# Kernel tuning notes

Measured on AMD Instinct MI355X. Metric: run time of the kernel, lower is better.

The kernel has to match this reference:

```python
import jax, jax.numpy as jnp
import numpy as np

B, T, C = 4, 2048, 2048
H, N = 32, 64          # n_head, head_size; H*N == C (n_dim_att == n_dim)
DMIX, DDEC = 32, 64    # hardcoded LoRA dims in module


def setup_inputs() -> dict:
    key = jax.random.key(0)
    ks = jax.random.split(key, 24)
    u = lambda k, s, lo, hi: jax.random.uniform(k, s, jnp.float32, lo, hi)
    g = lambda k, s: jax.random.normal(k, s, jnp.float32) * 0.02
    return {
        'x': jax.random.normal(ks[0], (B, T, C), jnp.float32),
        'shift_state_in': jax.random.normal(ks[1], (B, C), jnp.float32),
        'wkv_state_in': jnp.zeros((B, H, N, N), jnp.float32),
        'time_maa_x': u(ks[2], (C,), 0.0, 1.0),
        'time_maa_r': u(ks[3], (C,), 0.0, 1.0),
        'time_maa_k': u(ks[4], (C,), 0.0, 1.0),
        'time_maa_v': u(ks[5], (C,), 0.0, 1.0),
        'time_maa_w': u(ks[6], (C,), 0.0, 1.0),
        'time_maa_v2': u(ks[7], (C,), 0.0, 1.0),
        'time_maa_w1': u(ks[8], (C, DMIX * 5), -0.01, 0.01),
        'time_maa_w2': u(ks[9], (5, DMIX, C), -0.01, 0.01),
        'time_decay': u(ks[10], (C,), -6.0, -1.0),
        'time_decay_w1': u(ks[11], (C, DDEC), -0.01, 0.01),
        'time_decay_w2': u(ks[12], (DDEC, C), -0.01, 0.01),
        'time_value2_w1': u(ks[13], (C, DDEC), -0.01, 0.01),
        'time_value2_w2': u(ks[14], (DDEC, C), -0.01, 0.01),
        'W_r': g(ks[15], (C, C)),
        'W_k': g(ks[16], (C, C)),
        'W_v': g(ks[17], (C, C)),
        'W_o': g(ks[18], (C, C)),
        'ln_w': jnp.ones((C,), jnp.float32),
        'ln_b': jnp.zeros((C,), jnp.float32),
    }


def _to_heads(a):
    # [B,T,C] -> [T,B,H,N] for time-major scan
    return a.reshape(B, T, H, N).transpose(1, 0, 2, 3)


def reference(x, shift_state_in, wkv_state_in,
              time_maa_x, time_maa_r, time_maa_k, time_maa_v, time_maa_w, time_maa_v2,
              time_maa_w1, time_maa_w2,
              time_decay, time_decay_w1, time_decay_w2,
              time_value2_w1, time_value2_w2,
              W_r, W_k, W_v, W_o, ln_w, ln_b):
    # token shift
    dxprev = jnp.concatenate([shift_state_in[:, None, :], x[:, :-1]], axis=1) - x
    xxx = x + dxprev * time_maa_x
    hmix = jnp.tanh(xxx @ time_maa_w1).reshape(B, T, 5, DMIX)
    mix = jnp.einsum('btfd,fdc->fbtc', hmix, time_maa_w2)  # [5,B,T,C]
    mr, mk, mv, mw, mv2 = mix
    xr = x + dxprev * (time_maa_r + mr)
    xk = x + dxprev * (time_maa_k + mk)
    xv = x + dxprev * (time_maa_v + mv)
    xw = x + dxprev * (time_maa_w + mw)
    xv2 = x + dxprev * (time_maa_v2 + mv2)

    r = xr @ W_r
    k = xk @ W_k
    v = xv @ W_v
    v2 = xv2 @ W_v + jnp.tanh(xv2 @ time_value2_w1) @ time_value2_w2
    w = time_decay + jnp.tanh(xw @ time_decay_w1) @ time_decay_w2
    decay = jnp.exp(-jnp.exp(w))         # per-channel, data-dependent
    k = k * (1.0 - decay)

    rh, kh, vh, dh = _to_heads(r), _to_heads(k), _to_heads(v), _to_heads(decay)

    def step(state, inputs):
        # state: [B,H,N,N] (k-dim x v-dim); u (time_faaaa) is zero in this variant
        r_t, k_t, v_t, d_t = inputs  # each [B,H,N]
        y = jnp.einsum('bhi,bhij->bhj', r_t, state)
        state = state * d_t[..., None] + k_t[..., None] * v_t[..., None, :]
        return state, y

    wkv_state_out, ys = jax.lax.scan(step, wkv_state_in, (rh, kh, vh, dh))
    y = ys.transpose(1, 0, 2, 3).reshape(B, T, C)
    y = y + v2
    # LayerNorm over n_dim_att
    mu = jnp.mean(y, axis=-1, keepdims=True)
    var = jnp.var(y, axis=-1, keepdims=True)
    y = (y - mu) / jnp.sqrt(var + 1e-5) * ln_w + ln_b
    y = y @ W_o
    return y, x[:, -1], wkv_state_out
```

## Files before the change

kernel.cpp:

```cpp
#include <hip/hip_runtime.h>
#include <hip/hip_bf16.h>
#include <cstdio>


typedef __attribute__((ext_vector_type(8))) short bf16x8;
typedef __attribute__((ext_vector_type(4))) float floatx4;

#define T_DIM 2048
#define C_DIM 2048
#define B_DIM 4
#define M_ROWS (B_DIM * T_DIM)

typedef const unsigned int __attribute__((address_space(1)))* gas1_t;
typedef unsigned int __attribute__((address_space(3)))* las3_t;
__device__ __forceinline__ void gl_lds16(const void* g, void* l) {
    __builtin_amdgcn_global_load_lds((gas1_t)g, (las3_t)l, 16, 0, 0);
}

__global__ __launch_bounds__(256) void k_transpose(
    const float* __restrict__ in, void* __restrict__ out,
    int R, int Cin, int to_bf16)
{
    __shared__ float tile[32][33];
    const int tx = threadIdx.x & 31, ty = threadIdx.x >> 5;
    const int cbase = blockIdx.x * 32, rbase = blockIdx.y * 32;
#pragma unroll
    for (int i = 0; i < 4; i++) {
        int r = rbase + ty + i * 8;
        int c = cbase + tx;
        tile[ty + i * 8][tx] = (c < Cin) ? in[(size_t)r * Cin + c] : 0.0f;
    }
    __syncthreads();
    if (to_bf16) {
        __hip_bfloat16* ob = (__hip_bfloat16*)out;
#pragma unroll
        for (int i = 0; i < 4; i++) {
            int c = cbase + ty + i * 8;
            ob[(size_t)c * R + rbase + tx] = __float2bfloat16(tile[tx][ty + i * 8]);
        }
    } else {
        float* of = (float*)out;
#pragma unroll
        for (int i = 0; i < 4; i++) {
            int c = cbase + ty + i * 8;
            of[(size_t)c * R + rbase + tx] = tile[tx][ty + i * 8];
        }
    }
}

__global__ __launch_bounds__(256) void k_xx(
    const float* __restrict__ x, const float* __restrict__ shift,
    const float* __restrict__ tmx,
    __hip_bfloat16* __restrict__ XX, float* __restrict__ xlast)
{
    const int row = blockIdx.x;
    const int b = row >> 11, t = row & 2047;
    const int c0 = threadIdx.x * 8;
    const float* xrow = x + (size_t)row * C_DIM;
    const float* prow = (t == 0) ? (shift + (size_t)b * C_DIM) : (xrow - C_DIM);
    float4 xa = ((const float4*)(xrow + c0))[0];
    float4 xb = ((const float4*)(xrow + c0))[1];
    float4 pa = ((const float4*)(prow + c0))[0];
    float4 pb = ((const float4*)(prow + c0))[1];
    float xv8[8] = {xa.x, xa.y, xa.z, xa.w, xb.x, xb.y, xb.z, xb.w};
    float pv8[8] = {pa.x, pa.y, pa.z, pa.w, pb.x, pb.y, pb.z, pb.w};
    union { bf16x8 v8; __hip_bfloat16 e[8]; } u;
#pragma unroll
    for (int j = 0; j < 8; j++)
        u.e[j] = __float2bfloat16(fmaf(pv8[j] - xv8[j], tmx[c0 + j], xv8[j]));
    *(bf16x8*)(XX + (size_t)row * C_DIM + c0) = u.v8;
    if (t == T_DIM - 1) {
        ((float4*)(xlast + (size_t)b * C_DIM + c0))[0] = xa;
        ((float4*)(xlast + (size_t)b * C_DIM + c0))[1] = xb;
    }
}

__global__ __launch_bounds__(256) void k_gemm_h(
    const __hip_bfloat16* __restrict__ A,
    const __hip_bfloat16* __restrict__ Bt,
    __hip_bfloat16* __restrict__ Hout)
{
    __shared__ __hip_bfloat16 As[64 * 32];
    __shared__ __hip_bfloat16 Bs[256 * 32];
    const int tid = threadIdx.x;
    const int m0 = blockIdx.x * 64;
    const int wave = tid >> 6, lane = tid & 63;
    const int fcol = lane & 15, quad = lane >> 4;
    floatx4 acc[16];
#pragma unroll
    for (int i = 0; i < 16; i++) acc[i] = (floatx4){0.f, 0.f, 0.f, 0.f};

    const int rA = tid >> 2, kcA = (tid & 3) * 8;
    const __hip_bfloat16* gA = A + (size_t)(m0 + rA) * 2048 + kcA;
    __hip_bfloat16* lA = As + tid * 8;
    const __hip_bfloat16* gB[4];
    __hip_bfloat16* lB[4];
#pragma unroll
    for (int s = 0; s < 4; s++) {
        int q = tid + 256 * s;
        gB[s] = Bt + (size_t)(q >> 2) * 2048 + (q & 3) * 8;
        lB[s] = Bs + q * 8;
    }
    for (int kk = 0; kk < 2048; kk += 32) {
        gl_lds16(gA + kk, lA);
#pragma unroll
        for (int s = 0; s < 4; s++) gl_lds16(gB[s] + kk, lB[s]);
        __syncthreads();
        bf16x8 aF = *(const bf16x8*)(As + (wave * 16 + fcol) * 32 + quad * 8);
#pragma unroll
        for (int ni = 0; ni < 16; ni++) {
            bf16x8 bF = *(const bf16x8*)(Bs + (ni * 16 + fcol) * 32 + quad * 8);
            acc[ni] = __builtin_amdgcn_mfma_f32_16x16x32_bf16(aF, bF, acc[ni], 0, 0, 0);
        }
        __syncthreads();
    }
#pragma unroll
    for (int ni = 0; ni < 16; ni++) {
        int col = ni * 16 + fcol;
#pragma unroll
        for (int g = 0; g < 4; g++) {
            int row = m0 + wave * 16 + quad * 4 + g;
            Hout[(size_t)row * 256 + col] = __float2bfloat16(tanhf(acc[ni][g]));
        }
    }
}

__global__ __launch_bounds__(256) void k_gemm_n64(
    const __hip_bfloat16* __restrict__ A,
    const __hip_bfloat16* __restrict__ Bt,
    __hip_bfloat16* __restrict__ G)
{
    __shared__ __hip_bfloat16 As[64 * 32];
    __shared__ __hip_bfloat16 Bs[64 * 32];
    const int tid = threadIdx.x;
    const int m0 = blockIdx.x * 64;
    const int wave = tid >> 6, lane = tid & 63;
    const int fcol = lane & 15, quad = lane >> 4;
    floatx4 acc[4];
#pragma unroll
    for (int i = 0; i < 4; i++) acc[i] = (floatx4){0.f, 0.f, 0.f, 0.f};

    const int r = tid >> 2, kc = (tid & 3) * 8;
    const __hip_bfloat16* gA = A + (size_t)(m0 + r) * 2048 + kc;
    const __hip_bfloat16* gB = Bt + (size_t)r * 2048 + kc;
    __hip_bfloat16* lA = As + tid * 8;
    __hip_bfloat16* lB = Bs + tid * 8;
    for (int kk = 0; kk < 2048; kk += 32) {
        gl_lds16(gA + kk, lA);
        gl_lds16(gB + kk, lB);
        __syncthreads();
        bf16x8 aF = *(const bf16x8*)(As + (wave * 16 + fcol) * 32 + quad * 8);
#pragma unroll
        for (int ni = 0; ni < 4; ni++) {
            bf16x8 bF = *(const bf16x8*)(Bs + (ni * 16 + fcol) * 32 + quad * 8);
            acc[ni] = __builtin_amdgcn_mfma_f32_16x16x32_bf16(aF, bF, acc[ni], 0, 0, 0);
        }
        __syncthreads();
    }
#pragma unroll
    for (int ni = 0; ni < 4; ni++) {
        int col = ni * 16 + fcol;
#pragma unroll
        for (int g = 0; g < 4; g++) {
            int row = m0 + wave * 16 + quad * 4 + g;
            G[(size_t)row * 64 + col] = __float2bfloat16(tanhf(acc[ni][g]));
        }
    }
}

__global__ __launch_bounds__(256) void k_mixfused(
    const float* __restrict__ x, const float* __restrict__ shift,
    const __hip_bfloat16* __restrict__ Hb,
    const __hip_bfloat16* __restrict__ w2T,
    const float* __restrict__ tmr, const float* __restrict__ tmk,
    const float* __restrict__ tmv, const float* __restrict__ tmw,
    const float* __restrict__ tmv2,
    __hip_bfloat16* __restrict__ xr, __hip_bfloat16* __restrict__ xk,
    __hip_bfloat16* __restrict__ xv, __hip_bfloat16* __restrict__ xw,
    __hip_bfloat16* __restrict__ xv2)
{
    __shared__ float          xp[33 * 256];
    __shared__ __hip_bfloat16 Hs[32 * 256];
    __shared__ __hip_bfloat16 mixS[32 * 256];

    const int tid = threadIdx.x;
    const int bid = blockIdx.x;
    const int n0 = (bid & 7) * 256;
    const int m0 = (bid >> 3) * 32;
    const int wave = tid >> 6, lane = tid & 63;
    const int fcol = lane & 15, quad = lane >> 4;
    const int wm = (wave >> 1) * 16, wn = (wave & 1) * 128;

#pragma unroll
    for (int i = 0; i < 8; i++) {
        int row = i * 4 + wave;
        gl_lds16(x + (size_t)(m0 + row) * C_DIM + n0 + lane * 4,
                 xp + (row + 1) * 256 + lane * 4);
    }
    if (wave == 0) {
        const float* src = (m0 & 2047)
            ? (x + (size_t)(m0 - 1) * C_DIM + n0)
            : (shift + (size_t)(m0 >> 11) * C_DIM + n0);
        gl_lds16(src + lane * 4, xp + lane * 4);
    }
#pragma unroll
    for (int i = 0; i < 4; i++) {
        int q = tid + 256 * i;
        gl_lds16(Hb + (size_t)(m0 + (q >> 5)) * 256 + (q & 31) * 8,
                 Hs + (q >> 5) * 256 + (q & 31) * 8);
    }
    asm volatile("s_waitcnt vmcnt(0) lgkmcnt(0)" ::: "memory");
    __builtin_amdgcn_s_barrier();
    __builtin_amdgcn_sched_barrier(0);

    const float* maas[5] = {tmr, tmk, tmv, tmw, tmv2};
    __hip_bfloat16* outs[5] = {xr, xk, xv, xw, xv2};
    const int cc = tid & 31, c0 = cc * 8, rb = tid >> 5;

#pragma unroll
    for (int f = 0; f < 5; f++) {
        {
            bf16x8 aF = *(const bf16x8*)(Hs + (wm + fcol) * 256 + f * 32 + quad * 8);
            floatx4 acc[8];
#pragma unroll
            for (int nf = 0; nf < 8; nf++) {
                bf16x8 bF = *(const bf16x8*)(
                    w2T + (size_t)(n0 + wn + nf * 16 + fcol) * 160 + f * 32 + quad * 8);
                acc[nf] = __builtin_amdgcn_mfma_f32_16x16x32_bf16(
                    aF, bF, (floatx4){0.f, 0.f, 0.f, 0.f}, 0, 0, 0);
            }
#pragma unroll
            for (int nf = 0; nf < 8; nf++)
#pragma unroll
                for (int g = 0; g < 4; g++)
                    mixS[(wm + quad * 4 + g) * 256 + wn + nf * 16 + fcol] =
                        __float2bfloat16(acc[nf][g]);
        }
        asm volatile("s_waitcnt lgkmcnt(0)" ::: "memory");
        __builtin_amdgcn_s_barrier();
        __builtin_amdgcn_sched_barrier(0);

        {
            float4 ma = ((const float4*)(maas[f] + n0 + c0))[0];
            float4 mb = ((const float4*)(maas[f] + n0 + c0))[1];
            float m8[8] = {ma.x, ma.y, ma.z, ma.w, mb.x, mb.y, mb.z, mb.w};
#pragma unroll
            for (int i = 0; i < 4; i++) {
                int row = rb + 8 * i;
                float4 xa = ((const float4*)(xp + (row + 1) * 256 + c0))[0];
                float4 xb = ((const float4*)(xp + (row + 1) * 256 + c0))[1];
                float4 pa = ((const float4*)(xp + row * 256 + c0))[0];
                float4 pb = ((const float4*)(xp + row * 256 + c0))[1];
                float xv8[8] = {xa.x, xa.y, xa.z, xa.w, xb.x, xb.y, xb.z, xb.w};
                float pv8[8] = {pa.x, pa.y, pa.z, pa.w, pb.x, pb.y, pb.z, pb.w};
                union { bf16x8 v8; __hip_bfloat16 e[8]; } mu;
                mu.v8 = *(const bf16x8*)(mixS + row * 256 + c0);
                union { bf16x8 v8; __hip_bfloat16 e[8]; } u;
#pragma unroll
                for (int j = 0; j < 8; j++) {
                    float dx = pv8[j] - xv8[j];
                    float mixv = __bfloat162float(mu.e[j]);
                    u.e[j] = __float2bfloat16(fmaf(dx, m8[j] + mixv, xv8[j]));
                }
                *(bf16x8*)(outs[f] + (size_t)(m0 + row) * C_DIM + n0 + c0) = u.v8;
            }
        }
        if (f < 4) {
            asm volatile("s_waitcnt lgkmcnt(0)" ::: "memory");
            __builtin_amdgcn_s_barrier();
            __builtin_amdgcn_sched_barrier(0);
        }
    }
}

__global__ __launch_bounds__(512, 2) void k_gemm256(
    const __hip_bfloat16* __restrict__ A,
    const __hip_bfloat16* __restrict__ Bt,
    int mode,
    float* __restrict__ outF, __hip_bfloat16* __restrict__ outB)
{
    constexpr int K = 2048;
    constexpr int NT = K / 32;
    __shared__ __hip_bfloat16 LA[4][256 * 32];
    __shared__ __hip_bfloat16 LB[4][256 * 32];
    const int tid = threadIdx.x;
    const int bid = blockIdx.x;
    const int n0 = (bid & 7) * 256;
    const int m0 = (bid >> 3) * 256;
    const int wave = tid >> 6, lane = tid & 63;
    const int wm = (wave >> 2) * 128, wn = (wave & 3) * 64;
    const int fcol = lane & 15, quad = lane >> 4;

    floatx4 acc[8][4];
#pragma unroll
    for (int mi = 0; mi < 8; mi++)
#pragma unroll
        for (int ni = 0; ni < 4; ni++)
            acc[mi][ni] = (floatx4){0.f, 0.f, 0.f, 0.f};

    const int ch0 = wave * 2, ch1 = wave * 2 + 1;
    const int rr = lane >> 2, kc = (lane & 3) * 8;
    const __hip_bfloat16* pA0 = A  + (size_t)(m0 + ch0 * 16 + rr) * K + kc;
    const __hip_bfloat16* pA1 = A  + (size_t)(m0 + ch1 * 16 + rr) * K + kc;
    const __hip_bfloat16* pB0 = Bt + (size_t)(n0 + ch0 * 16 + rr) * K + kc;
    const __hip_bfloat16* pB1 = Bt + (size_t)(n0 + ch1 * 16 + rr) * K + kc;
    const int lo0 = ch0 * 512 + lane * 8;
    const int lo1 = ch1 * 512 + lane * 8;

    int ns = 0;
    for (; ns < 3; ++ns) {
        gl_lds16(pA0 + ns * 32, &LA[ns][lo0]);
        gl_lds16(pA1 + ns * 32, &LA[ns][lo1]);
        gl_lds16(pB0 + ns * 32, &LB[ns][lo0]);
        gl_lds16(pB1 + ns * 32, &LB[ns][lo1]);
    }
    for (int t = 0; t < NT; ++t) {
        if (t < NT - 2)       asm volatile("s_waitcnt vmcnt(8)" ::: "memory");
        else if (t == NT - 2) asm volatile("s_waitcnt vmcnt(4)" ::: "memory");
        else                  asm volatile("s_waitcnt vmcnt(0)" ::: "memory");
        asm volatile("s_barrier" ::: "memory");
        if (ns < NT) {
            const int sl = ns & 3;
            gl_lds16(pA0 + ns * 32, &LA[sl][lo0]);
            gl_lds16(pA1 + ns * 32, &LA[sl][lo1]);
            gl_lds16(pB0 + ns * 32, &LB[sl][lo0]);
            gl_lds16(pB1 + ns * 32, &LB[sl][lo1]);
            ++ns;
        }
        const int st = t & 3;
        const __hip_bfloat16* ab = &LA[st][(wm + fcol) * 32 + quad * 8];
        const __hip_bfloat16* bb = &LB[st][(wn + fcol) * 32 + quad * 8];
        bf16x8 bF[4];
#pragma unroll
        for (int ni = 0; ni < 4; ni++)
            bF[ni] = *(const bf16x8*)(bb + ni * 512);
#pragma unroll
        for (int mi = 0; mi < 8; mi++) {
            bf16x8 aF = *(const bf16x8*)(ab + mi * 512);
#pragma unroll
            for (int ni = 0; ni < 4; ni++)
                acc[mi][ni] = __builtin_amdgcn_mfma_f32_16x16x32_bf16(
                    aF, bF[ni], acc[mi][ni], 0, 0, 0);
        }
    }
#pragma unroll
    for (int mi = 0; mi < 8; mi++) {
#pragma unroll
        for (int ni = 0; ni < 4; ni++) {
            int rbase = m0 + wm + mi * 16 + quad * 4;
            int ccol = n0 + wn + ni * 16 + fcol;
#pragma unroll
            for (int g = 0; g < 4; g++) {
                size_t idx = (size_t)(rbase + g) * 2048 + ccol;
                float val = acc[mi][ni][g];
                if (mode == 0) outF[idx] = val;
                else           outB[idx] = __float2bfloat16(val);
            }
        }
    }
}

__global__ __launch_bounds__(256) void k_gemm64(
    const __hip_bfloat16* __restrict__ A0, const __hip_bfloat16* __restrict__ B0,
    const __hip_bfloat16* __restrict__ A1, const __hip_bfloat16* __restrict__ B1,
    float* __restrict__ decayOut, const float* __restrict__ tdec,
    __hip_bfloat16* __restrict__ v2Out)
{
    constexpr int K = 64;
    __shared__ __hip_bfloat16 As[128 * 32];
    __shared__ __hip_bfloat16 Bs[128 * 32];
    const int tid = threadIdx.x;
    const int op = blockIdx.x >> 10;
    const int id = blockIdx.x & 1023;
    const int xcd = id & 7, jj = id >> 3;
    const int m0 = (((xcd << 3) | (jj & 7))) * 128;
    const int n0 = (jj >> 3) * 128;
    const __hip_bfloat16* A = op ? A1 : A0;
    const __hip_bfloat16* Bt = op ? B1 : B0;
    const int wave = tid >> 6, lane = tid & 63;
    const int wm = (wave >> 1) * 64, wn = (wave & 1) * 64;
    const int fcol = lane & 15, quad = lane >> 4;

    floatx4 acc[4][4];
#pragma unroll
    for (int mi = 0; mi < 4; mi++)
#pragma unroll
        for (int ni = 0; ni < 4; ni++)
            acc[mi][ni] = (floatx4){0.f, 0.f, 0.f, 0.f};

    const int q0 = tid, q1 = tid + 256;
    const int r0 = q0 >> 2, kc0 = (q0 & 3) * 8;
    const int r1 = q1 >> 2, kc1 = (q1 & 3) * 8;
    const __hip_bfloat16* gA0 = A + (size_t)(m0 + r0) * K + kc0;
    const __hip_bfloat16* gA1 = A + (size_t)(m0 + r1) * K + kc1;
    const __hip_bfloat16* gB0 = Bt + (size_t)(n0 + r0) * K + kc0;
    const __hip_bfloat16* gB1 = Bt + (size_t)(n0 + r1) * K + kc1;
    __hip_bfloat16* lA0 = As + q0 * 8; __hip_bfloat16* lA1 = As + q1 * 8;
    __hip_bfloat16* lB0 = Bs + q0 * 8; __hip_bfloat16* lB1 = Bs + q1 * 8;

    for (int kk = 0; kk < K; kk += 32) {
        gl_lds16(gA0 + kk, lA0);
        gl_lds16(gA1 + kk, lA1);
        gl_lds16(gB0 + kk, lB0);
        gl_lds16(gB1 + kk, lB1);
        __syncthreads();
        bf16x8 aF[4], bF[4];
#pragma unroll
        for (int mi = 0; mi < 4; mi++)
            aF[mi] = *(const bf16x8*)(As + (wm + mi * 16 + fcol) * 32 + quad * 8);
#pragma unroll
        for (int ni = 0; ni < 4; ni++)
            bF[ni] = *(const bf16x8*)(Bs + (wn + ni * 16 + fcol) * 32 + quad * 8);
#pragma unroll
        for (int mi = 0; mi < 4; mi++)
#pragma unroll
            for (int ni = 0; ni < 4; ni++)
                acc[mi][ni] = __builtin_amdgcn_mfma_f32_16x16x32_bf16(
                    aF[mi], bF[ni], acc[mi][ni], 0, 0, 0);
        __syncthreads();
    }
#pragma unroll
    for (int mi = 0; mi < 4; mi++) {
#pragma unroll
        for (int ni = 0; ni < 4; ni++) {
            int rbase = m0 + wm + mi * 16 + quad * 4;
            int ccol = n0 + wn + ni * 16 + fcol;
#pragma unroll
            for (int g = 0; g < 4; g++) {
                size_t idx = (size_t)(rbase + g) * 2048 + ccol;
                float val = acc[mi][ni][g];
                if (op == 0) {
                    decayOut[idx] = expf(-expf(val + tdec[ccol]));
                } else {
                    v2Out[idx] = __float2bfloat16(__bfloat162float(v2Out[idx]) + val);
                }
            }
        }
    }
}

__global__ __launch_bounds__(512) void k_scan_chunked(
    const __hip_bfloat16* __restrict__ r, const __hip_bfloat16* __restrict__ k,
    const __hip_bfloat16* __restrict__ v, const float* __restrict__ dec,
    const float* __restrict__ state_in,
    __hip_bfloat16* __restrict__ y, float* __restrict__ state_out)
{
    __shared__ __hip_bfloat16 Rs[2][64 * 64];
    __shared__ __hip_bfloat16 Ks[2][64 * 64];
    __shared__ __hip_bfloat16 Vs[2][64 * 64];
    __shared__ float          Dsb[2][64 * 64];
    __shared__ __hip_bfloat16 Ys[2][64 * 64];
    __shared__ __hip_bfloat16 Am[64 * 72];
    __shared__ __hip_bfloat16 Bm[64 * 72];
    __shared__ __hip_bfloat16 VT[64 * 72];
    __shared__ __hip_bfloat16 CT[64 * 72];
    __shared__ __hip_bfloat16 ST[64 * 72];
    __shared__ __hip_bfloat16 Pm[64 * 72];
    __shared__ float part[8][64];
    __shared__ float efin[64];

    const int tid = threadIdx.x;
    const int bh = blockIdx.x, b = bh >> 5, h = bh & 31;
    const int wave = tid >> 6, lane = tid & 63;
    const int fcol = lane & 15, quad = lane >> 4;
    const int wr = wave & 3, wc = wave >> 2;
    const int ci = lane, seg = wave;

    floatx4 sfr[2];
    {
        const float* sp = state_in + (size_t)bh * 4096;
#pragma unroll
        for (int n = 0; n < 2; n++)
#pragma unroll
            for (int g = 0; g < 4; g++)
                sfr[n][g] = sp[(size_t)(16 * wr + quad * 4 + g) * 64
                               + 32 * wc + 16 * n + fcol];
    }

    const size_t cbase0 = (size_t)b * T_DIM * C_DIM + (size_t)h * 64;

    auto stage = [&](int cc, int buf) {
        const size_t cb = cbase0 + (size_t)cc * 64 * C_DIM;
        const size_t o = (size_t)(tid >> 3) * C_DIM + (tid & 7) * 8;
        gl_lds16(r + cb + o, &Rs[buf][tid * 8]);
        gl_lds16(k + cb + o, &Ks[buf][tid * 8]);
        gl_lds16(v + cb + o, &Vs[buf][tid * 8]);
        gl_lds16(y + cb + o, &Ys[buf][tid * 8]);
#pragma unroll
        for (int s = 0; s < 2; s++) {
            int q = tid + 512 * s;
            gl_lds16(dec + cb + (size_t)(q >> 4) * C_DIM + (q & 15) * 4,
                     &Dsb[buf][q * 4]);
        }
    };

    stage(0, 0);

    for (int c = 0; c < 32; c++) {
        const int cur = c & 1, nxt = cur ^ 1;
        const size_t cb = cbase0 + (size_t)c * 64 * C_DIM;

        if (c == 0) asm volatile("s_waitcnt vmcnt(0)" ::: "memory");
        else        asm volatile("s_waitcnt vmcnt(8)" ::: "memory");
        asm volatile("s_waitcnt lgkmcnt(0)" ::: "memory");
        __builtin_amdgcn_s_barrier();
        __builtin_amdgcn_sched_barrier(0);

        if (c + 1 < 32) stage(c + 1, nxt);

        {
#pragma unroll
            for (int n = 0; n < 2; n++)
#pragma unroll
                for (int g = 0; g < 4; g++)
                    ST[(size_t)(32 * wc + 16 * n + fcol) * 72
                       + 16 * wr + quad * 4 + g] = __float2bfloat16(sfr[n][g]);
            float p = 1.0f;
#pragma unroll
            for (int u = 0; u < 8; u++) p *= Dsb[cur][(seg * 8 + u) * 64 + ci];
            part[seg][ci] = p;
        }
        asm volatile("s_waitcnt lgkmcnt(0)" ::: "memory");
        __builtin_amdgcn_s_barrier();
        __builtin_amdgcn_sched_barrier(0);

        {
            float pp[8];
#pragma unroll
            for (int s = 0; s < 8; s++) pp[s] = part[s][ci];
            float pre = 1.0f;
#pragma unroll
            for (int s = 0; s < 7; s++) pre *= (s < seg) ? pp[s] : 1.0f;
            float tot = pp[0] * pp[1] * pp[2] * pp[3]
                      * pp[4] * pp[5] * pp[6] * pp[7];
            if (seg == 0) efin[ci] = tot;
            float e = pre;
#pragma unroll
            for (int u = 0; u < 8; u++) {
                int t = seg * 8 + u;
                float d = Dsb[cur][t * 64 + ci];
                float rv = __bfloat162float(Rs[cur][t * 64 + ci]);
                float kv = __bfloat162float(Ks[cur][t * 64 + ci]) * (1.0f - d);
                Am[t * 72 + ci] = __float2bfloat16(rv * e);
                e *= d;
                float bb = kv * __builtin_amdgcn_rcpf(e);
                Bm[t * 72 + ci] = __float2bfloat16(bb);
                CT[ci * 72 + t] = __float2bfloat16(bb * tot);
            }
#pragma unroll
            for (int u = 0; u < 8; u++) {
                int t = seg * 8 + ((u + (ci & 7)) & 7);
                VT[ci * 72 + t] = Vs[cur][t * 64 + ci];
            }
        }
        asm volatile("s_waitcnt lgkmcnt(0)" ::: "memory");
        __builtin_amdgcn_s_barrier();
        __builtin_amdgcn_sched_barrier(0);

        {
            bf16x8 af[2];
#pragma unroll
            for (int kk = 0; kk < 2; kk++)
                af[kk] = *(const bf16x8*)(Am + (16 * wr + fcol) * 72 + kk * 32 + quad * 8);
            floatx4 pfr[4];
#pragma unroll
            for (int n4 = 0; n4 < 4; n4++) {
                pfr[n4] = (floatx4){0.f, 0.f, 0.f, 0.f};
#pragma unroll
                for (int kk = 0; kk < 2; kk++) {
                    bf16x8 bF = *(const bf16x8*)(Bm + (16 * n4 + fcol) * 72 + kk * 32 + quad * 8);
                    pfr[n4] = __builtin_amdgcn_mfma_f32_16x16x32_bf16(af[kk], bF, pfr[n4], 0, 0, 0);
                }
            }
            floatx4 yfr[2];
#pragma unroll
            for (int n = 0; n < 2; n++) {
                yfr[n] = (floatx4){0.f, 0.f, 0.f, 0.f};
#pragma unroll
                for (int kk = 0; kk < 2; kk++) {
                    bf16x8 sF = *(const bf16x8*)(ST + (32 * wc + 16 * n + fcol) * 72 + kk * 32 + quad * 8);
                    yfr[n] = __builtin_amdgcn_mfma_f32_16x16x32_bf16(af[kk], sF, yfr[n], 0, 0, 0);
                }
            }
#pragma unroll
            for (int n4 = 0; n4 < 4; n4++)
#pragma unroll
                for (int g = 0; g < 4; g++) {
                    int t = 16 * wr + quad * 4 + g;
                    int s = 16 * n4 + fcol;
                    Pm[t * 72 + s] = (s < t) ? __float2bfloat16(pfr[n4][g])
                                             : __float2bfloat16(0.0f);
                }
            float eg[4];
#pragma unroll
            for (int g = 0; g < 4; g++) eg[g] = efin[16 * wr + quad * 4 + g];
#pragma unroll
            for (int n = 0; n < 2; n++)
#pragma unroll
                for (int g = 0; g < 4; g++) sfr[n][g] *= eg[g];
            bf16x8 pf[2], cf[2];
#pragma unroll
            for (int kk = 0; kk < 2; kk++) {
                pf[kk] = *(const bf16x8*)(Pm + (16 * wr + fcol) * 72 + kk * 32 + quad * 8);
                cf[kk] = *(const bf16x8*)(CT + (16 * wr + fcol) * 72 + kk * 32 + quad * 8);
            }
#pragma unroll
            for (int n = 0; n < 2; n++) {
#pragma unroll
                for (int kk = 0; kk < 2; kk++) {
                    bf16x8 vF = *(const bf16x8*)(VT + (32 * wc + 16 * n + fcol) * 72 + kk * 32 + quad * 8);
                    yfr[n] = __builtin_amdgcn_mfma_f32_16x16x32_bf16(pf[kk], vF, yfr[n], 0, 0, 0);
                    sfr[n] = __builtin_amdgcn_mfma_f32_16x16x32_bf16(cf[kk], vF, sfr[n], 0, 0, 0);
                }
            }
#pragma unroll
            for (int n = 0; n < 2; n++)
#pragma unroll
                for (int g = 0; g < 4; g++) {
                    int t = 16 * wr + quad * 4 + g;
                    int j = 32 * wc + 16 * n + fcol;
                    size_t addr = cb + (size_t)t * C_DIM + j;
                    float yv = __bfloat162float(Ys[cur][t * 64 + j]) + yfr[n][g];
                    y[addr] = __float2bfloat16(yv);
                }
        }
    }
    {
        float* so = state_out + (size_t)bh * 4096;
#pragma unroll
        for (int n = 0; n < 2; n++)
#pragma unroll
            for (int g = 0; g < 4; g++)
                so[(size_t)(16 * wr + quad * 4 + g) * 64 + 32 * wc + 16 * n + fcol]
                    = sfr[n][g];
    }
}

__global__ __launch_bounds__(256) void k_addln(
    __hip_bfloat16* __restrict__ y,
    const float* __restrict__ lnw, const float* __restrict__ lnb)
{
    __shared__ float ls[4], ls2[4];
    const int row = blockIdx.x;
    const size_t base = (size_t)row * C_DIM;
    const int tid = threadIdx.x;
    const int c0 = tid * 8;
    union { bf16x8 v8; __hip_bfloat16 e[8]; } uin;
    uin.v8 = *(const bf16x8*)(y + base + c0);
    float vbuf[8];
#pragma unroll
    for (int j = 0; j < 8; j++) vbuf[j] = __bfloat162float(uin.e[j]);
    float s = 0.f, s2 = 0.f;
#pragma unroll
    for (int j = 0; j < 8; j++) { s += vbuf[j]; s2 += vbuf[j] * vbuf[j]; }
#pragma unroll
    for (int off = 32; off > 0; off >>= 1) {
        s += __shfl_down(s, off, 64);
        s2 += __shfl_down(s2, off, 64);
    }
    const int w = tid >> 6;
    if ((tid & 63) == 0) { ls[w] = s; ls2[w] = s2; }
    __syncthreads();
    float S = ls[0] + ls[1] + ls[2] + ls[3];
    float S2 = ls2[0] + ls2[1] + ls2[2] + ls2[3];
    float mu = S * (1.0f / C_DIM);
    float var = S2 * (1.0f / C_DIM) - mu * mu;
    float rs = rsqrtf(var + 1e-5f);
    union { bf16x8 v8; __hip_bfloat16 e[8]; } u;
#pragma unroll
    for (int j = 0; j < 8; j++) {
        int ccc = c0 + j;
        u.e[j] = __float2bfloat16((vbuf[j] - mu) * rs * lnw[ccc] + lnb[ccc]);
    }
    *(bf16x8*)(y + base + c0) = u.v8;
}

extern "C" void kernel_launch(void* const* d_in, const int* in_sizes, int n_in,
                              void* d_out, int out_size, void* d_ws, size_t ws_size,
                              hipStream_t stream)
{
    const float* x     = (const float*)d_in[0];
    const float* shift = (const float*)d_in[1];
    const float* wkvin = (const float*)d_in[2];
    const float* tmx   = (const float*)d_in[3];
    const float* tmr   = (const float*)d_in[4];
    const float* tmk   = (const float*)d_in[5];
    const float* tmv   = (const float*)d_in[6];
    const float* tmw   = (const float*)d_in[7];
    const float* tmv2  = (const float*)d_in[8];
    const float* w1    = (const float*)d_in[9];
    const float* w2    = (const float*)d_in[10];
    const float* tdec  = (const float*)d_in[11];
    const float* dw1   = (const float*)d_in[12];
    const float* dw2   = (const float*)d_in[13];
    const float* vw1   = (const float*)d_in[14];
    const float* vw2   = (const float*)d_in[15];
    const float* Wr    = (const float*)d_in[16];
    const float* Wk    = (const float*)d_in[17];
    const float* Wv    = (const float*)d_in[18];
    const float* Wo    = (const float*)d_in[19];
    const float* lnw   = (const float*)d_in[20];
    const float* lnb   = (const float*)d_in[21];

    const size_t SZ_XBF = (size_t)M_ROWS * C_DIM * 2;
    const size_t SZ_WBF = (size_t)C_DIM * C_DIM * 2;
    char* ws = (char*)d_ws;
    size_t off = 0;
    __hip_bfloat16* S0 = (__hip_bfloat16*)(ws + off); off += SZ_XBF;
    __hip_bfloat16* S1 = (__hip_bfloat16*)(ws + off); off += SZ_XBF;
    __hip_bfloat16* S2 = (__hip_bfloat16*)(ws + off); off += SZ_XBF;
    __hip_bfloat16* S3 = (__hip_bfloat16*)(ws + off); off += SZ_XBF;
    __hip_bfloat16* S4 = (__hip_bfloat16*)(ws + off); off += SZ_XBF;
    char* D = ws + off; off += (size_t)M_ROWS * C_DIM * 4;
    __hip_bfloat16* XX    = (__hip_bfloat16*)D;
    __hip_bfloat16* Hb    = (__hip_bfloat16*)(D + SZ_XBF);
    float*          decay = (float*)D;
    __hip_bfloat16* WrT = (__hip_bfloat16*)(ws + off); off += SZ_WBF;
    __hip_bfloat16* WkT = (__hip_bfloat16*)(ws + off); off += SZ_WBF;
    __hip_bfloat16* WvT = (__hip_bfloat16*)(ws + off); off += SZ_WBF;
    __hip_bfloat16* WoT = (__hip_bfloat16*)(ws + off); off += SZ_WBF;
    __hip_bfloat16* w1tb  = (__hip_bfloat16*)(ws + off); off += (size_t)256 * 2048 * 2;
    __hip_bfloat16* dw1t  = (__hip_bfloat16*)(ws + off); off += (size_t)64 * 2048 * 2;
    __hip_bfloat16* vw1t  = (__hip_bfloat16*)(ws + off); off += (size_t)64 * 2048 * 2;
    __hip_bfloat16* dw2t  = (__hip_bfloat16*)(ws + off); off += (size_t)2048 * 64 * 2;
    __hip_bfloat16* vw2t  = (__hip_bfloat16*)(ws + off); off += (size_t)2048 * 64 * 2;
    __hip_bfloat16* Gd    = (__hip_bfloat16*)(ws + off); off += (size_t)M_ROWS * 64 * 2;
    __hip_bfloat16* Gv    = (__hip_bfloat16*)(ws + off); off += (size_t)M_ROWS * 64 * 2;
    __hip_bfloat16* w2T   = (__hip_bfloat16*)(ws + off); off += (size_t)2048 * 160 * 2;
    if (ws_size < off) {
        fprintf(stderr, "kernel_launch: ws too small (%zu < %zu)\n", ws_size, off);
        return;
    }

    float* out_y     = (float*)d_out;
    float* out_xlast = out_y + (size_t)M_ROWS * C_DIM;
    float* out_state = out_xlast + (size_t)B_DIM * C_DIM;

    k_transpose<<<dim3(8, 64),  256, 0, stream>>>(w1,  w1tb, 2048, 160, 1);
    k_transpose<<<dim3(2, 64),  256, 0, stream>>>(dw1, dw1t, 2048, 64, 1);
    k_transpose<<<dim3(2, 64),  256, 0, stream>>>(vw1, vw1t, 2048, 64, 1);
    k_transpose<<<dim3(64, 2),  256, 0, stream>>>(dw2, dw2t, 64, 2048, 1);
    k_transpose<<<dim3(64, 2),  256, 0, stream>>>(vw2, vw2t, 64, 2048, 1);
    k_transpose<<<dim3(64, 5),  256, 0, stream>>>(w2,  w2T,  160, 2048, 1);
    k_transpose<<<dim3(64, 64), 256, 0, stream>>>(Wr, WrT, 2048, 2048, 1);
    k_transpose<<<dim3(64, 64), 256, 0, stream>>>(Wk, WkT, 2048, 2048, 1);
    k_transpose<<<dim3(64, 64), 256, 0, stream>>>(Wv, WvT, 2048, 2048, 1);
    k_transpose<<<dim3(64, 64), 256, 0, stream>>>(Wo, WoT, 2048, 2048, 1);

    k_xx<<<M_ROWS, 256, 0, stream>>>(x, shift, tmx, XX, out_xlast);
    k_gemm_h<<<128, 256, 0, stream>>>(XX, w1tb, Hb);
    k_mixfused<<<2048, 256, 0, stream>>>(x, shift, Hb, w2T,
                                         tmr, tmk, tmv, tmw, tmv2,
                                         S0, S1, S2, S3, S4);
    k_gemm_n64<<<128, 256, 0, stream>>>(S3, dw1t, Gd);
    k_gemm_n64<<<128, 256, 0, stream>>>(S4, vw1t, Gv);
    k_gemm256<<<256, 512, 0, stream>>>(S1, WkT, 1, nullptr, S3);
    k_gemm256<<<256, 512, 0, stream>>>(S0, WrT, 1, nullptr, S1);
    k_gemm256<<<256, 512, 0, stream>>>(S2, WvT, 1, nullptr, S0);
    k_gemm256<<<256, 512, 0, stream>>>(S4, WvT, 1, nullptr, S2);
    k_gemm64<<<2048, 256, 0, stream>>>(Gd, dw2t, Gv, vw2t, decay, tdec, S2);
    k_scan_chunked<<<128, 512, 0, stream>>>(S1, S3, S0, decay, wkvin, S2, out_state);
    k_addln<<<M_ROWS, 256, 0, stream>>>(S2, lnw, lnb);
    k_gemm256<<<256, 512, 0, stream>>>(S2, WoT, 0, out_y, nullptr);

    (void)in_sizes; (void)n_in; (void)out_size;
}
```

Before: 1.117 ms.

## Rewrite 256x256 GEMM main loop with K=64 tiles, swizzled LDS, and staggered staging

The big bf16 GEMM kernel moves from a 4-stage K=32 ring buffer to a 2-stage K=64 double buffer with an XOR-swizzled LDS layout to avoid bank conflicts. Each iteration is split into four MFMA quadrants separated by barriers, and the A and B half-tile global-to-LDS loads for later iterations are interleaved between them. Wave priority is raised around MFMA bursts. The aim is better overlap of memory and compute and fewer LDS conflicts, at the cost of more barriers per iteration and tricky vmcnt accounting.

```diff
diff --git a/kernel.cpp b/kernel.cpp
--- a/kernel.cpp
+++ b/kernel.cpp
@@ -280,9 +280,9 @@
     float* __restrict__ outF, __hip_bfloat16* __restrict__ outB)
 {
     constexpr int K = 2048;
-    constexpr int NT = K / 32;
-    __shared__ __hip_bfloat16 LA[4][256 * 32];
-    __shared__ __hip_bfloat16 LB[4][256 * 32];
+    constexpr int NT = K / 64;
+    __shared__ __hip_bfloat16 LA[2][16384];
+    __shared__ __hip_bfloat16 LB[2][16384];
     const int tid = threadIdx.x;
     const int bid = blockIdx.x;
     const int n0 = (bid & 7) * 256;
@@ -298,51 +298,126 @@
         for (int ni = 0; ni < 4; ni++)
             acc[mi][ni] = (floatx4){0.f, 0.f, 0.f, 0.f};
 
-    const int ch0 = wave * 2, ch1 = wave * 2 + 1;
-    const int rr = lane >> 2, kc = (lane & 3) * 8;
-    const __hip_bfloat16* pA0 = A  + (size_t)(m0 + ch0 * 16 + rr) * K + kc;
-    const __hip_bfloat16* pA1 = A  + (size_t)(m0 + ch1 * 16 + rr) * K + kc;
-    const __hip_bfloat16* pB0 = Bt + (size_t)(n0 + ch0 * 16 + rr) * K + kc;
-    const __hip_bfloat16* pB1 = Bt + (size_t)(n0 + ch1 * 16 + rr) * K + kc;
-    const int lo0 = ch0 * 512 + lane * 8;
-    const int lo1 = ch1 * 512 + lane * 8;
-
-    int ns = 0;
-    for (; ns < 3; ++ns) {
-        gl_lds16(pA0 + ns * 32, &LA[ns][lo0]);
-        gl_lds16(pA1 + ns * 32, &LA[ns][lo1]);
-        gl_lds16(pB0 + ns * 32, &LB[ns][lo0]);
-        gl_lds16(pB1 + ns * 32, &LB[ns][lo1]);
-    }
+    const int srow = tid >> 3;
+    const int kqe  = ((tid & 7) ^ (srow & 7)) * 8;
+    const __hip_bfloat16* gA = A  + (size_t)(m0 + srow) * K + kqe;
+    const __hip_bfloat16* gB = Bt + (size_t)(n0 + srow) * K + kqe;
+
+    auto stageA = [&](int tau) {
+        __hip_bfloat16* l = &LA[tau & 1][0] + tid * 8;
+        const __hip_bfloat16* g = gA + tau * 64;
+        gl_lds16(g,                  l);
+        gl_lds16(g + (size_t)64*K,   l + 4096);
+        gl_lds16(g + (size_t)128*K,  l + 8192);
+        gl_lds16(g + (size_t)192*K,  l + 12288);
+    };
+    auto stageBlo = [&](int tau) {
+        __hip_bfloat16* l = &LB[tau & 1][0] + tid * 8;
+        const __hip_bfloat16* g = gB + tau * 64;
+        gl_lds16(g,                 l);
+        gl_lds16(g + (size_t)64*K,  l + 4096);
+    };
+    auto stageBhi = [&](int tau) {
+        __hip_bfloat16* l = &LB[tau & 1][0] + 8192 + tid * 8;
+        const __hip_bfloat16* g = gB + (size_t)128*K + tau * 64;
+        gl_lds16(g,                 l);
+        gl_lds16(g + (size_t)64*K,  l + 4096);
+    };
+
+    const int swz0 = (quad ^ (fcol & 7)) * 8;
+    const int swz1 = swz0 ^ 32;
+    const int aOff = (wm >> 7) * 8192 + fcol * 64;
+    const int bOff = (wn >> 7) * 8192 + (wn & 127) * 64 + fcol * 64;
+
+    stageA(0); stageBlo(0); stageBhi(0); stageA(1);
+    asm volatile("s_waitcnt vmcnt(4)" ::: "memory");
+
+    bf16x8 a[4][2], b0[2][2], b1[2][2];
     for (int t = 0; t < NT; ++t) {
-        if (t < NT - 2)       asm volatile("s_waitcnt vmcnt(8)" ::: "memory");
-        else if (t == NT - 2) asm volatile("s_waitcnt vmcnt(4)" ::: "memory");
-        else                  asm volatile("s_waitcnt vmcnt(0)" ::: "memory");
-        asm volatile("s_barrier" ::: "memory");
-        if (ns < NT) {
-            const int sl = ns & 3;
-            gl_lds16(pA0 + ns * 32, &LA[sl][lo0]);
-            gl_lds16(pA1 + ns * 32, &LA[sl][lo1]);
-            gl_lds16(pB0 + ns * 32, &LB[sl][lo0]);
-            gl_lds16(pB1 + ns * 32, &LB[sl][lo1]);
-            ++ns;
-        }
-        const int st = t & 3;
-        const __hip_bfloat16* ab = &LA[st][(wm + fcol) * 32 + quad * 8];
-        const __hip_bfloat16* bb = &LB[st][(wn + fcol) * 32 + quad * 8];
-        bf16x8 bF[4];
-#pragma unroll
-        for (int ni = 0; ni < 4; ni++)
-            bF[ni] = *(const bf16x8*)(bb + ni * 512);
-#pragma unroll
-        for (int mi = 0; mi < 8; mi++) {
-            bf16x8 aF = *(const bf16x8*)(ab + mi * 512);
-#pragma unroll
-            for (int ni = 0; ni < 4; ni++)
-                acc[mi][ni] = __builtin_amdgcn_mfma_f32_16x16x32_bf16(
-                    aF, bF[ni], acc[mi][ni], 0, 0, 0);
-        }
-    }
+        const int d = t & 1;
+        const __hip_bfloat16* ab = &LA[d][0] + aOff;
+        const __hip_bfloat16* bb = &LB[d][0] + bOff;
+
+        __builtin_amdgcn_s_barrier();
+        __builtin_amdgcn_sched_barrier(0);
+#pragma unroll
+        for (int mi = 0; mi < 4; mi++) {
+            a[mi][0] = *(const bf16x8*)(ab + mi * 1024 + swz0);
+            a[mi][1] = *(const bf16x8*)(ab + mi * 1024 + swz1);
+        }
+#pragma unroll
+        for (int ni = 0; ni < 2; ni++) {
+            b0[ni][0] = *(const bf16x8*)(bb + ni * 1024 + swz0);
+            b0[ni][1] = *(const bf16x8*)(bb + ni * 1024 + swz1);
+        }
+        if (t + 1 < NT) stageBlo(t + 1);
+        __builtin_amdgcn_s_setprio(1);
+#pragma unroll
+        for (int mi = 0; mi < 4; mi++)
+#pragma unroll
+            for (int ni = 0; ni < 2; ni++) {
+                acc[mi][ni] = __builtin_amdgcn_mfma_f32_16x16x32_bf16(a[mi][0], b0[ni][0], acc[mi][ni], 0, 0, 0);
+                acc[mi][ni] = __builtin_amdgcn_mfma_f32_16x16x32_bf16(a[mi][1], b0[ni][1], acc[mi][ni], 0, 0, 0);
+            }
+        __builtin_amdgcn_s_setprio(0);
+
+        __builtin_amdgcn_s_barrier();
+        __builtin_amdgcn_sched_barrier(0);
+#pragma unroll
+        for (int ni = 0; ni < 2; ni++) {
+            b1[ni][0] = *(const bf16x8*)(bb + (2 + ni) * 1024 + swz0);
+            b1[ni][1] = *(const bf16x8*)(bb + (2 + ni) * 1024 + swz1);
+        }
+        if (t + 1 < NT) stageBhi(t + 1);
+        __builtin_amdgcn_s_setprio(1);
+#pragma unroll
+        for (int mi = 0; mi < 4; mi++)
+#pragma unroll
+            for (int ni = 0; ni < 2; ni++) {
+                acc[mi][2 + ni] = __builtin_amdgcn_mfma_f32_16x16x32_bf16(a[mi][0], b1[ni][0], acc[mi][2 + ni], 0, 0, 0);
+                acc[mi][2 + ni] = __builtin_amdgcn_mfma_f32_16x16x32_bf16(a[mi][1], b1[ni][1], acc[mi][2 + ni], 0, 0, 0);
+            }
+        __builtin_amdgcn_s_setprio(0);
+
+        __builtin_amdgcn_s_barrier();
+        __builtin_amdgcn_sched_barrier(0);
+#pragma unroll
+        for (int mi = 0; mi < 4; mi++) {
+            a[mi][0] = *(const bf16x8*)(ab + (4 + mi) * 1024 + swz0);
+            a[mi][1] = *(const bf16x8*)(ab + (4 + mi) * 1024 + swz1);
+        }
+        __builtin_amdgcn_s_setprio(1);
+#pragma unroll
+        for (int mi = 0; mi < 4; mi++)
+#pragma unroll
+            for (int ni = 0; ni < 2; ni++) {
+                acc[4 + mi][2 + ni] = __builtin_amdgcn_mfma_f32_16x16x32_bf16(a[mi][0], b1[ni][0], acc[4 + mi][2 + ni], 0, 0, 0);
+                acc[4 + mi][2 + ni] = __builtin_amdgcn_mfma_f32_16x16x32_bf16(a[mi][1], b1[ni][1], acc[4 + mi][2 + ni], 0, 0, 0);
+            }
+        __builtin_amdgcn_s_setprio(0);
+
+        __builtin_amdgcn_s_barrier();
+        __builtin_amdgcn_sched_barrier(0);
+#pragma unroll
+        for (int ni = 0; ni < 2; ni++) {
+            b0[ni][0] = *(const bf16x8*)(bb + ni * 1024 + swz0);
+            b0[ni][1] = *(const bf16x8*)(bb + ni * 1024 + swz1);
+        }
+        if (t + 2 < NT) stageA(t + 2);
+        __builtin_amdgcn_s_setprio(1);
+#pragma unroll
+        for (int mi = 0; mi < 4; mi++)
+#pragma unroll
+            for (int ni = 0; ni < 2; ni++) {
+                acc[4 + mi][ni] = __builtin_amdgcn_mfma_f32_16x16x32_bf16(a[mi][0], b0[ni][0], acc[4 + mi][ni], 0, 0, 0);
+                acc[4 + mi][ni] = __builtin_amdgcn_mfma_f32_16x16x32_bf16(a[mi][1], b0[ni][1], acc[4 + mi][ni], 0, 0, 0);
+            }
+        __builtin_amdgcn_s_setprio(0);
+
+        if (t < NT - 2)       asm volatile("s_waitcnt vmcnt(4)" ::: "memory");
+        else if (t == NT - 2) asm volatile("s_waitcnt vmcnt(0)" ::: "memory");
+    }
+
 #pragma unroll
     for (int mi = 0; mi < 8; mi++) {
 #pragma unroll
```

Result: faster. 1.083 ms (-3.1%).
